# Kernel tuning notes

Hardware: AMD Instinct MI355X
Metric: run time of the kernel (lower is better)

Reference implementation:

```python
import jax, jax.numpy as jnp
import numpy as np

B, N = 2, 6
C_IN, C_OUT, D = 256, 80, 16
HF, WF = 32, 88
H_IN, W_IN = 256, 704
BEV_H, BEV_W = 128, 128
X_MIN, Y_MIN, Z_MIN, X_MAX, Y_MAX, Z_MAX = -51.2, -51.2, -5.0, 51.2, 51.2, 3.0
D_MIN, D_MAX = 0.0, 45.0
DX = (X_MAX - X_MIN) / BEV_W
DY = (Y_MAX - Y_MIN) / BEV_H


def _make_cameras():
    # Plausible surround-view rig: P = K [R|t], last row [0,0,0,1]
    K = np.array([[600., 0., W_IN / 2.], [0., 600., H_IN / 2.], [0., 0., 1.]])
    P = np.array([[0., -1., 0.], [0., 0., -1.], [1., 0., 0.]])  # lidar axes -> cam axes
    l2i = np.zeros((B, N, 4, 4), np.float32)
    for b in range(B):
        for n in range(N):
            th = 2 * np.pi * n / N + 0.05 * b
            Rz = np.array([[np.cos(-th), -np.sin(-th), 0.],
                           [np.sin(-th), np.cos(-th), 0.],
                           [0., 0., 1.]])
            Rc = P @ Rz
            c = np.array([1.5 * np.cos(th), 1.5 * np.sin(th), 1.6])  # camera center in lidar frame
            t = -Rc @ c
            M = np.eye(4)
            M[:3, :3] = K @ Rc
            M[:3, 3] = K @ t
            l2i[b, n] = M
    return jnp.asarray(l2i, dtype=jnp.float32)


def _make_aug():
    A = np.tile(np.eye(4, dtype=np.float32), (B, N, 1, 1))
    A[..., 0, 0] = 0.95
    A[..., 1, 1] = 0.95
    A[..., 0, 3] = 4.0
    A[..., 1, 3] = 2.0
    return jnp.asarray(A)


def setup_inputs() -> dict:
    key = jax.random.key(0)
    k = jax.random.split(key, 4)
    x = jax.random.normal(k[0], (B, N, C_IN, HF, WF), jnp.float32)
    w_dep = jax.random.normal(k[1], (D + C_OUT, C_IN), jnp.float32) * (1.0 / np.sqrt(C_IN))
    b_dep = jnp.zeros((D + C_OUT,), jnp.float32)
    w_ref = jax.random.normal(k[2], (C_OUT, C_OUT, 3, 3), jnp.float32) * (1.0 / np.sqrt(9.0 * C_OUT))
    b_ref = jnp.zeros((C_OUT,), jnp.float32)
    return {"x": x, "lidar2img": _make_cameras(), "img_aug": _make_aug(),
            "w_dep": w_dep, "b_dep": b_dep, "w_ref": w_ref, "b_ref": b_ref}


def _forward(x, lidar2img, img_aug, w_dep, b_dep, w_ref, b_ref):
    BN = B * N
    HW = HF * WF
    xf = x.reshape(BN, C_IN, HF, WF)
    # depthnet head: 1x1 conv -> D depth logits + C_OUT context channels
    y = jnp.einsum('oc,bchw->bohw', w_dep, xf) + b_dep[None, :, None, None]
    depth = jax.nn.softmax(y[:, :D], axis=1).reshape(BN, D, HW)   # (BN,D,HW)
    ctx = y[:, D:].reshape(BN, C_OUT, HW)                          # (BN,C,HW)

    # pixel-center grid in network-input image coords (as _make_pixel_grid)
    us = (jnp.arange(WF, dtype=jnp.float32) + 0.5) * (W_IN / WF)
    vs = (jnp.arange(HF, dtype=jnp.float32) + 0.5) * (H_IN / HF)
    vv, uu = jnp.meshgrid(vs, us, indexing='ij')
    uv1 = jnp.stack([uu, vv, jnp.ones_like(uu)], -1).reshape(HW, 3)

    # undo image augmentation: uv_raw = post_rot^-1 (uv1 - post_tran)
    aug = img_aug.reshape(BN, 4, 4)
    inv_rot = jnp.linalg.inv(aug[:, :3, :3])
    uv_raw = jnp.einsum('bij,bpj->bpi', inv_rot, uv1[None] - aug[:, None, :3, 3])  # (BN,HW,3)

    # unproject: X_lidar = lidar2img^-1 @ [u*d, v*d, d, 1]  (== R^-1(K^-1 d uv - t))
    inv_l2i = jnp.linalg.inv(lidar2img.reshape(BN, 4, 4))
    dvals = D_MIN + (jnp.arange(D, dtype=jnp.float32) + 0.5) * ((D_MAX - D_MIN) / D)
    pts_h = uv_raw[:, None, :, :] * dvals[None, :, None, None]                     # (BN,D,HW,3)
    pts = jnp.einsum('bij,bdpj->bdpi', inv_l2i[:, :3, :3], pts_h) + inv_l2i[:, None, None, :3, 3]

    ix = jnp.floor((pts[..., 0] - X_MIN) / DX).astype(jnp.int32)
    iy = jnp.floor((pts[..., 1] - Y_MIN) / DY).astype(jnp.int32)
    valid = (ix >= 0) & (ix < BEV_W) & (iy >= 0) & (iy < BEV_H) & \
            (pts[..., 2] >= Z_MIN) & (pts[..., 2] < Z_MAX)                          # (BN,D,HW)

    bidx = (jnp.arange(BN, dtype=jnp.int32) // N)[:, None, None]
    NUM = B * BEV_H * BEV_W
    flat = bidx * (BEV_H * BEV_W) + iy * BEV_W + ix
    flat = jnp.where(valid, flat, NUM).reshape(-1)  # invalid -> dump bucket

    # lift: per-point feature = depth_prob * context  -> splat (scatter-add) into BEV
    feat = depth[:, :, :, None] * jnp.swapaxes(ctx, 1, 2)[:, None, :, :]            # (BN,D,HW,C)
    acc = jax.ops.segment_sum(feat.reshape(-1, C_OUT), flat, num_segments=NUM + 1)[:NUM]
    cnt = jax.ops.segment_sum(jnp.ones_like(flat, dtype=jnp.float32), flat, num_segments=NUM + 1)[:NUM]
    acc = acc / jnp.maximum(cnt, 1.0)[:, None]  # normalize=True: average over points per cell

    bev = acc.reshape(B, BEV_H, BEV_W, C_OUT).transpose(0, 3, 1, 2)                 # (B,C,H,W)
    out = jax.lax.conv_general_dilated(bev, w_ref, (1, 1), 'SAME',
                                       dimension_numbers=('NCHW', 'OIHW', 'NCHW'))
    return out + b_ref[None, :, None, None]


def reference(x, lidar2img, img_aug, w_dep, b_dep, w_ref, b_ref):
    return _forward(x, lidar2img, img_aug, w_dep, b_dep, w_ref, b_ref)
```

## Files before the change

### kernel.cpp

```cpp
#include <hip/hip_runtime.h>
#include <math.h>

namespace {
constexpr int B_   = 2;
constexpr int NCAM = 6;
constexpr int BN   = 12;
constexpr int CIN  = 256;
constexpr int COUT = 80;
constexpr int DBIN = 16;
constexpr int NOUT = 96;
constexpr int HF = 32, WF = 88;
constexpr int HW = HF * WF;
constexpr int BEVH = 128, BEVW = 128;
constexpr int NUMC = B_ * BEVH * BEVW;
constexpr int NPTS = BN * DBIN * HW;

constexpr size_t MATS_OFF   = 0;
constexpr size_t WHI_OFF    = 2048;
constexpr size_t WLO_OFF    = WHI_OFF + 49152;
constexpr size_t YT_OFF     = 102400;
constexpr size_t CELL_OFF   = YT_OFF + 12976128;
constexpr size_t COUNTS_OFF = CELL_OFF + 2162688;
constexpr size_t STARTS_OFF = COUNTS_OFF + 131072;
constexpr size_t CURS_OFF   = STARTS_OFF + 131584;
constexpr size_t PLIST_OFF  = CURS_OFF + 131072;
constexpr size_t PCELL_OFF  = PLIST_OFF + 2162688;
constexpr size_t BEVHWC_OFF = PCELL_OFF + 2162688;
constexpr size_t WRH_OFF    = BEVHWC_OFF + 10485760;
constexpr size_t WRL_OFF    = WRH_OFF + 138240;
}

using bf16x8 = __attribute__((ext_vector_type(8))) short;
using f32x4  = __attribute__((ext_vector_type(4))) float;

__device__ inline unsigned short bf16rne(float f) {
    unsigned u = __float_as_uint(f);
    unsigned r = (u + 0x7FFFu + ((u >> 16) & 1u)) >> 16;
    return (unsigned short)r;
}

template<int NM>
__device__ void inv_lu_f32(float* A, float* Y) {
    int piv[NM];
    for (int j = 0; j < NM; j++) {
        int p = j; float mx = fabsf(A[j*NM+j]);
        for (int i = j+1; i < NM; i++) { float v = fabsf(A[i*NM+j]); if (v > mx) { mx = v; p = i; } }
        piv[j] = p;
        if (p != j) for (int k = 0; k < NM; k++) { float t = A[j*NM+k]; A[j*NM+k] = A[p*NM+k]; A[p*NM+k] = t; }
        float r = __fdiv_rn(1.0f, A[j*NM+j]);
        for (int i = j+1; i < NM; i++) A[i*NM+j] = __fmul_rn(A[i*NM+j], r);
        for (int i = j+1; i < NM; i++) {
            float lij = A[i*NM+j];
            for (int k = j+1; k < NM; k++)
                A[i*NM+k] = __fsub_rn(A[i*NM+k], __fmul_rn(lij, A[j*NM+k]));
        }
    }
    for (int c = 0; c < NM; c++) {
        float x[NM];
        for (int i = 0; i < NM; i++) x[i] = 0.f;
        x[c] = 1.f;
        for (int j = 0; j < NM; j++) { int p = piv[j]; if (p != j) { float t = x[j]; x[j] = x[p]; x[p] = t; } }
        for (int k = 0; k < NM; k++) {
            float xk = x[k];
            for (int i = k+1; i < NM; i++) x[i] = __fsub_rn(x[i], __fmul_rn(xk, A[i*NM+k]));
        }
        for (int k = NM-1; k >= 0; k--) {
            float xk = __fdiv_rn(x[k], A[k*NM+k]);
            x[k] = xk;
            for (int i = 0; i < k; i++) x[i] = __fsub_rn(x[i], __fmul_rn(xk, A[i*NM+k]));
        }
        for (int i = 0; i < NM; i++) Y[i*NM+c] = x[i];
    }
}

__global__ void lss_prep_kernel(const float* __restrict__ l2i,
                                const float* __restrict__ aug,
                                float* __restrict__ mats) {
    int n = threadIdx.x;
    if (n >= BN) return;
    float A[16], IA[16];
    for (int i = 0; i < 16; i++) A[i] = l2i[n*16 + i];
    inv_lu_f32<4>(A, IA);
    float R[9], IR[9];
    for (int i = 0; i < 3; i++)
        for (int j = 0; j < 3; j++) R[i*3+j] = aug[n*16 + i*4 + j];
    inv_lu_f32<3>(R, IR);
    float* o = mats + n*24;
    for (int i = 0; i < 9; i++) o[i] = IR[i];
    o[9]  = aug[n*16 + 3];
    o[10] = aug[n*16 + 7];
    o[11] = aug[n*16 + 11];
    for (int i = 0; i < 3; i++)
        for (int j = 0; j < 3; j++) o[12 + i*3 + j] = IA[i*4 + j];
    o[21] = IA[3]; o[22] = IA[7]; o[23] = IA[11];
}

__global__ void lss_wt_kernel(const float* __restrict__ w_dep,
                              unsigned short* __restrict__ wHi,
                              unsigned short* __restrict__ wLo) {
    int idx = blockIdx.x * 256 + threadIdx.x;
    float f = w_dep[idx];
    unsigned short h = bf16rne(f);
    float hf = __uint_as_float((unsigned)h << 16);
    wHi[idx] = h;
    wLo[idx] = bf16rne(f - hf);
}

__global__ void lss_wref_kernel(const float* __restrict__ w_ref,
                                unsigned short* __restrict__ wrh,
                                unsigned short* __restrict__ wrl) {
    int idx = blockIdx.x * 256 + threadIdx.x;
    int o  = idx / 864;
    int k  = idx - o * 864;
    int s  = k / 96;
    int ci = k - s * 96;
    float f = (ci < COUT) ? w_ref[(size_t)(o * COUT + ci) * 9 + s] : 0.f;
    unsigned short h = bf16rne(f);
    float hf = __uint_as_float((unsigned)h << 16);
    wrh[idx] = h;
    wrl[idx] = bf16rne(f - hf);
}

__global__ void lss_geom_kernel(const float* __restrict__ mats,
                                int* __restrict__ cellid,
                                int* __restrict__ counts) {
    int gp = blockIdx.x * 256 + threadIdx.x;
    int lane = threadIdx.x & 63;
    int bn = gp / HW, p = gp % HW;
    const float* m = mats + bn * 24;
    int ph = p / WF, pw = p % WF;
    float u = ((float)pw + 0.5f) * 8.0f;
    float v = ((float)ph + 0.5f) * 8.0f;
    float q0 = __fsub_rn(u, m[9]);
    float q1 = __fsub_rn(v, m[10]);
    float q2 = __fsub_rn(1.0f, m[11]);
    float r0 = __fadd_rn(__fadd_rn(__fmul_rn(m[0], q0), __fmul_rn(m[1], q1)), __fmul_rn(m[2], q2));
    float r1 = __fadd_rn(__fadd_rn(__fmul_rn(m[3], q0), __fmul_rn(m[4], q1)), __fmul_rn(m[5], q2));
    float r2 = __fadd_rn(__fadd_rn(__fmul_rn(m[6], q0), __fmul_rn(m[7], q1)), __fmul_rn(m[8], q2));
    int b = bn / NCAM;
    for (int d = 0; d < DBIN; d++) {
        float dv = __fmul_rn((float)d + 0.5f, 2.8125f);
        float p0 = __fmul_rn(r0, dv);
        float p1 = __fmul_rn(r1, dv);
        float p2 = __fmul_rn(r2, dv);
        float px = __fadd_rn(__fadd_rn(__fadd_rn(__fmul_rn(m[12], p0), __fmul_rn(m[13], p1)), __fmul_rn(m[14], p2)), m[21]);
        float py = __fadd_rn(__fadd_rn(__fadd_rn(__fmul_rn(m[15], p0), __fmul_rn(m[16], p1)), __fmul_rn(m[17], p2)), m[22]);
        float pz = __fadd_rn(__fadd_rn(__fadd_rn(__fmul_rn(m[18], p0), __fmul_rn(m[19], p1)), __fmul_rn(m[20], p2)), m[23]);
        float fx = floorf(__fdiv_rn(__fsub_rn(px, -51.2f), 0.8f));
        float fy = floorf(__fdiv_rn(__fsub_rn(py, -51.2f), 0.8f));
        int cell = -1;
        if (fx >= 0.0f && fx < 128.0f && fy >= 0.0f && fy < 128.0f && pz >= -5.0f && pz < 3.0f)
            cell = b * (BEVH * BEVW) + (int)fy * BEVW + (int)fx;
        cellid[(bn * DBIN + d) * HW + p] = cell;
        int cprev = __shfl_up(cell, 1);
        bool leader = (lane == 0) || (cell != cprev);
        unsigned long long L = __ballot(leader);
        unsigned long long above = (lane == 63) ? 0ull : (L >> (lane + 1));
        int runlen = above ? __ffsll(above) : (64 - lane);
        if (leader && cell >= 0) atomicAdd(&counts[cell], runlen);
    }
}

__global__ void lss_scan_kernel(const int* __restrict__ counts,
                                int* __restrict__ starts,
                                int* __restrict__ cursors) {
    __shared__ int sums[1024];
    int tid = threadIdx.x;
    int base = tid * 32;
    int local[32];
    int s = 0;
    #pragma unroll
    for (int i = 0; i < 32; i++) { local[i] = s; s += counts[base + i]; }
    sums[tid] = s;
    __syncthreads();
    for (int off = 1; off < 1024; off <<= 1) {
        int v = 0;
        if (tid >= off) v = sums[tid - off];
        __syncthreads();
        if (tid >= off) sums[tid] += v;
        __syncthreads();
    }
    int offset = (tid > 0) ? sums[tid - 1] : 0;
    #pragma unroll
    for (int i = 0; i < 32; i++) {
        int st = offset + local[i];
        starts[base + i]  = st;
        cursors[base + i] = st;
    }
    if (tid == 1023) starts[NUMC] = sums[1023];
}

__global__ void lss_fill_kernel(const int* __restrict__ cellid,
                                int* __restrict__ cursors,
                                int* __restrict__ plist,
                                int* __restrict__ pcell) {
    int i = blockIdx.x * 256 + threadIdx.x;
    int lane = threadIdx.x & 63;
    int c = cellid[i];
    int bn  = i / (DBIN * HW);
    int rem = i % (DBIN * HW);
    int d   = rem / HW;
    int p   = rem % HW;
    int pf  = ((bn * HW + p) << 4) | d;
    int cprev = __shfl_up(c, 1);
    bool leader = (lane == 0) || (c != cprev);
    unsigned long long L = __ballot(leader);
    unsigned long long above = (lane == 63) ? 0ull : (L >> (lane + 1));
    int runlen = above ? __ffsll(above) : (64 - lane);
    unsigned long long below = L & (~0ull >> (63 - lane));
    int lead = 63 - __clzll(below);
    int rank = lane - lead;
    int bse = 0;
    if (leader && c >= 0) bse = atomicAdd(&cursors[c], runlen);
    bse = __shfl(bse, lead);
    if (c >= 0) {
        plist[bse + rank] = pf;
        pcell[bse + rank] = c;
    }
}

__global__ __launch_bounds__(256) void lss_gemm_kernel(const float* __restrict__ x,
                                                       const unsigned short* __restrict__ wHi,
                                                       const unsigned short* __restrict__ wLo,
                                                       const float* __restrict__ b_dep,
                                                       float* __restrict__ yT) {
    __shared__ unsigned short xs[2][64][72];
    __shared__ unsigned short wsb[2][96][72];

    int tid  = threadIdx.x;
    int tl   = tid & 63;
    int tc   = tid >> 6;
    int pxg0 = blockIdx.x * 64;
    int bn   = pxg0 / HW;
    const float* xcol = x + (size_t)bn * CIN * HW + (pxg0 % HW) + tl;

    f32x4 acc[6];
    #pragma unroll
    for (int t = 0; t < 6; t++) acc[t] = (f32x4){0.f, 0.f, 0.f, 0.f};

    int lane = tid & 63;
    int wv   = tc;
    int n16  = lane & 15;
    int q    = lane >> 4;

    for (int k0 = 0; k0 < CIN; k0 += 64) {
        if (k0) __syncthreads();
        #pragma unroll 4
        for (int i = 0; i < 16; i++) {
            int kk = 4 * i + tc;
            float v = xcol[(size_t)(k0 + kk) * HW];
            unsigned short h = bf16rne(v);
            float hf = __uint_as_float((unsigned)h << 16);
            xs[0][tl][kk] = h;
            xs[1][tl][kk] = bf16rne(v - hf);
        }
        #pragma unroll
        for (int i = 0; i < 12; i++) {
            int idx = tid + i * 256;
            int plane = idx / 1536;
            int rem   = idx - plane * 1536;
            int o     = rem >> 4;
            int j     = rem & 15;
            const unsigned short* src = (plane ? wLo : wHi) + o * 256 + k0 + 4 * j;
            *(uint2*)&wsb[plane][o][4 * j] = *(const uint2*)src;
        }
        __syncthreads();
        #pragma unroll
        for (int ks = 0; ks < 64; ks += 32) {
            bf16x8 ah = *(const bf16x8*)&xs[0][16 * wv + n16][q * 8 + ks];
            bf16x8 al = *(const bf16x8*)&xs[1][16 * wv + n16][q * 8 + ks];
            #pragma unroll
            for (int t = 0; t < 6; t++) {
                bf16x8 bh = *(const bf16x8*)&wsb[0][16 * t + n16][q * 8 + ks];
                bf16x8 bl = *(const bf16x8*)&wsb[1][16 * t + n16][q * 8 + ks];
                acc[t] = __builtin_amdgcn_mfma_f32_16x16x32_bf16(ah, bh, acc[t], 0, 0, 0);
                acc[t] = __builtin_amdgcn_mfma_f32_16x16x32_bf16(ah, bl, acc[t], 0, 0, 0);
                acc[t] = __builtin_amdgcn_mfma_f32_16x16x32_bf16(al, bh, acc[t], 0, 0, 0);
            }
        }
    }

    float bias[6];
    #pragma unroll
    for (int t = 0; t < 6; t++) bias[t] = b_dep[16 * t + n16];
    #pragma unroll
    for (int r = 0; r < 4; r++) {
        int pxg = pxg0 + 16 * wv + 4 * q + r;
        float* yp = yT + (size_t)pxg * NOUT;
        float v0 = acc[0][r] + bias[0];
        float mx = v0;
        #pragma unroll
        for (int m = 1; m < 16; m <<= 1) mx = fmaxf(mx, __shfl_xor(mx, m));
        float e = expf(v0 - mx);
        float s = e;
        #pragma unroll
        for (int m = 1; m < 16; m <<= 1) s += __shfl_xor(s, m);
        yp[n16] = e / s;
        #pragma unroll
        for (int t = 1; t < 6; t++) yp[16 * t + n16] = acc[t][r] + bias[t];
    }
}

__global__ __launch_bounds__(256) void lss_gather_kernel(const float* __restrict__ yT,
                                                         const int* __restrict__ plist,
                                                         const int* __restrict__ pcell,
                                                         const int* __restrict__ nvptr,
                                                         float* __restrict__ bevHWC) {
    int wv   = threadIdx.x >> 6;
    int lane = threadIdx.x & 63;
    int pos0 = (blockIdx.x * 4 + wv) * 64;
    int nv = *nvptr;
    if (pos0 >= nv) return;
    int n = min(64, nv - pos0);
    int gp = pos0 + lane;
    int myp = (gp < nv) ? plist[gp] : 0;
    int myc = (gp < nv) ? pcell[gp] : -1;
    int l16 = lane & 15;

    float a0 = 0.f, a1 = 0.f;
    int cur = __shfl(myc, 0);
    int j = 0;
    for (; j + 4 <= n; j += 4) {
        int   pf[4], cc[4];
        float av[4], bv[4], dv[4];
        #pragma unroll
        for (int u = 0; u < 4; u++) {
            pf[u] = __shfl(myp, j + u);
            cc[u] = __shfl(myc, j + u);
        }
        #pragma unroll
        for (int u = 0; u < 4; u++) {
            const float* rp = yT + (size_t)(pf[u] >> 4) * NOUT;
            av[u] = rp[16 + lane];
            bv[u] = rp[80 + l16];
            dv[u] = rp[pf[u] & 15];
        }
        #pragma unroll
        for (int u = 0; u < 4; u++) {
            if (cc[u] != cur) {
                atomicAdd(&bevHWC[(size_t)cur * COUT + lane], a0);
                if (lane < 16) atomicAdd(&bevHWC[(size_t)cur * COUT + 64 + lane], a1);
                a0 = a1 = 0.f;
                cur = cc[u];
            }
            a0 = fmaf(dv[u], av[u], a0);
            a1 = fmaf(dv[u], bv[u], a1);
        }
    }
    for (; j < n; j++) {
        int pf = __shfl(myp, j);
        int c  = __shfl(myc, j);
        const float* rp = yT + (size_t)(pf >> 4) * NOUT;
        float aval = rp[16 + lane];
        float bval = rp[80 + l16];
        float dep  = rp[pf & 15];
        if (c != cur) {
            atomicAdd(&bevHWC[(size_t)cur * COUT + lane], a0);
            if (lane < 16) atomicAdd(&bevHWC[(size_t)cur * COUT + 64 + lane], a1);
            a0 = a1 = 0.f;
            cur = c;
        }
        a0 = fmaf(dep, aval, a0);
        a1 = fmaf(dep, bval, a1);
    }
    atomicAdd(&bevHWC[(size_t)cur * COUT + lane], a0);
    if (lane < 16) atomicAdd(&bevHWC[(size_t)cur * COUT + 64 + lane], a1);
}

__global__ __launch_bounds__(256) void lss_tr_kernel(const float* __restrict__ bevHWC,
                                                     const int* __restrict__ counts,
                                                     float* __restrict__ bevCHW) {
    __shared__ float t[COUT][65];
    __shared__ float ic[64];
    int tid = threadIdx.x;
    int cellbase = blockIdx.x * 64;
    if (tid < 64) {
        int cnt = counts[cellbase + tid];
        ic[tid] = 1.f / fmaxf((float)cnt, 1.f);
    }
    const float* src = bevHWC + (size_t)cellbase * COUT;
    #pragma unroll
    for (int k = 0; k < 20; k++) {
        int idx = tid + k * 256;
        int yx = idx / COUT, ch = idx % COUT;
        t[ch][yx] = src[idx];
    }
    __syncthreads();
    int b  = cellbase >> 14;
    int yx0 = cellbase & 16383;
    #pragma unroll
    for (int k = 0; k < 20; k++) {
        int idx = tid + k * 256;
        int ch = idx / 64, yxl = idx % 64;
        bevCHW[((size_t)(b * COUT + ch)) * (BEVH * BEVW) + yx0 + yxl] = t[ch][yxl] * ic[yxl];
    }
}

__global__ __launch_bounds__(256) void lss_conv_kernel(const float* __restrict__ bev,
                                                       const unsigned short* __restrict__ wrh,
                                                       const unsigned short* __restrict__ wrl,
                                                       const float* __restrict__ bias,
                                                       float* __restrict__ out) {
    __shared__ unsigned short inT[2][10][10][104];
    int tid = threadIdx.x;
    int blk = blockIdx.x;
    int b   = blk >> 8;
    int y0  = ((blk >> 4) & 15) * 8;
    int x0  = (blk & 15) * 8;
    int lane = tid & 63, w = tid >> 6;
    int q = lane >> 4, n16 = lane & 15;
    int ow = w >> 1;
    int pj = (w & 1) * 2;
    int pr = n16 >> 3, pc = n16 & 7;
    int NO = ow ? 2 : 3;
    int obase = ow * 48;
    int kq = 8 * q;
    int rowb0 = 2 * pj + pr;

    int woff[3];
    #pragma unroll
    for (int i = 0; i < 3; i++) woff[i] = (obase + 16 * i + n16) * 864 + kq;

    f32x4 acc[3][2];
    #pragma unroll
    for (int i = 0; i < 3; i++)
        #pragma unroll
        for (int j = 0; j < 2; j++) acc[i][j] = (f32x4){0.f, 0.f, 0.f, 0.f};

    const float* pb = bev + (size_t)b * COUT * (BEVH * BEVW);

    for (int cc = 0; cc < 3; cc++) {
        int ci0 = cc * 32;
        if (cc) __syncthreads();
        #pragma unroll
        for (int t = 0; t < 13; t++) {
            int idx = tid + t * 256;
            if (idx < 3200) {
                int ci  = idx / 100;
                int rem = idx - ci * 100;
                int r   = rem / 10;
                int c   = rem - r * 10;
                int gy = y0 + r - 1, gx = x0 + c - 1;
                int gci = ci0 + ci;
                float v = 0.f;
                if (gy >= 0 && gy < BEVH && gx >= 0 && gx < BEVW && gci < COUT)
                    v = pb[((size_t)gci * BEVH + gy) * BEVW + gx];
                unsigned short h = bf16rne(v);
                float hf = __uint_as_float((unsigned)h << 16);
                inT[0][r][c][ci] = h;
                inT[1][r][c][ci] = bf16rne(v - hf);
            }
        }
        __syncthreads();
        #pragma unroll
        for (int s = 0; s < 9; s++) {
            int dy = s / 3, dx = s - dy * 3;
            int kb = s * 96 + ci0;
            bf16x8 bh[2], bl[2];
            #pragma unroll
            for (int j = 0; j < 2; j++) {
                int rr = rowb0 + 2 * j + dy;
                int ccol = pc + dx;
                bh[j] = *(const bf16x8*)&inT[0][rr][ccol][kq];
                bl[j] = *(const bf16x8*)&inT[1][rr][ccol][kq];
            }
            #pragma unroll
            for (int i = 0; i < 3; i++) {
                if (i < NO) {
                    bf16x8 ah = *(const bf16x8*)&wrh[woff[i] + kb];
                    bf16x8 al = *(const bf16x8*)&wrl[woff[i] + kb];
                    #pragma unroll
                    for (int j = 0; j < 2; j++) {
                        acc[i][j] = __builtin_amdgcn_mfma_f32_16x16x32_bf16(ah, bh[j], acc[i][j], 0, 0, 0);
                        acc[i][j] = __builtin_amdgcn_mfma_f32_16x16x32_bf16(ah, bl[j], acc[i][j], 0, 0, 0);
                        acc[i][j] = __builtin_amdgcn_mfma_f32_16x16x32_bf16(al, bh[j], acc[i][j], 0, 0, 0);
                    }
                }
            }
        }
    }
    #pragma unroll
    for (int i = 0; i < 3; i++) {
        if (i < NO) {
            #pragma unroll
            for (int j = 0; j < 2; j++) {
                int gy = y0 + 2 * (pj + j) + pr;
                int gx = x0 + pc;
                #pragma unroll
                for (int r = 0; r < 4; r++) {
                    int o = obase + 16 * i + 4 * q + r;
                    out[((size_t)(b * COUT + o) * BEVH + gy) * BEVW + gx] = acc[i][j][r] + bias[o];
                }
            }
        }
    }
}

extern "C" void kernel_launch(void* const* d_in, const int* in_sizes, int n_in,
                              void* d_out, int out_size, void* d_ws, size_t ws_size,
                              hipStream_t stream) {
    (void)in_sizes; (void)n_in; (void)out_size; (void)ws_size;
    const float* x     = (const float*)d_in[0];
    const float* l2i   = (const float*)d_in[1];
    const float* aug   = (const float*)d_in[2];
    const float* w_dep = (const float*)d_in[3];
    const float* b_dep = (const float*)d_in[4];
    const float* w_ref = (const float*)d_in[5];
    const float* b_ref = (const float*)d_in[6];
    float* out = (float*)d_out;

    char* ws = (char*)d_ws;
    float* mats    = (float*)(ws + MATS_OFF);
    unsigned short* wHi = (unsigned short*)(ws + WHI_OFF);
    unsigned short* wLo = (unsigned short*)(ws + WLO_OFF);
    unsigned short* wrh = (unsigned short*)(ws + WRH_OFF);
    unsigned short* wrl = (unsigned short*)(ws + WRL_OFF);
    float* yT      = (float*)(ws + YT_OFF);
    float* bevCHW  = (float*)(ws + YT_OFF);
    int*   cellid  = (int*)(ws + CELL_OFF);
    int*   counts  = (int*)(ws + COUNTS_OFF);
    int*   starts  = (int*)(ws + STARTS_OFF);
    int*   cursors = (int*)(ws + CURS_OFF);
    int*   plist   = (int*)(ws + PLIST_OFF);
    int*   pcell   = (int*)(ws + PCELL_OFF);
    float* bevHWC  = (float*)(ws + BEVHWC_OFF);

    hipMemsetAsync(counts, 0, NUMC * sizeof(int), stream);
    hipMemsetAsync(bevHWC, 0, (size_t)NUMC * COUT * sizeof(float), stream);
    lss_prep_kernel<<<1, 64, 0, stream>>>(l2i, aug, mats);
    lss_wt_kernel<<<96, 256, 0, stream>>>(w_dep, wHi, wLo);
    lss_wref_kernel<<<270, 256, 0, stream>>>(w_ref, wrh, wrl);
    lss_geom_kernel<<<BN * HW / 256, 256, 0, stream>>>(mats, cellid, counts);
    lss_scan_kernel<<<1, 1024, 0, stream>>>(counts, starts, cursors);
    lss_fill_kernel<<<NPTS / 256, 256, 0, stream>>>(cellid, cursors, plist, pcell);
    lss_gemm_kernel<<<528, 256, 0, stream>>>(x, wHi, wLo, b_dep, yT);
    lss_gather_kernel<<<NPTS / 256, 256, 0, stream>>>(yT, plist, pcell, starts + NUMC, bevHWC);
    lss_tr_kernel<<<NUMC / 64, 256, 0, stream>>>(bevHWC, counts, bevCHW);
    lss_conv_kernel<<<512, 256, 0, stream>>>(bevCHW, wrh, wrl, b_ref, out);
}
```

Measured before the change: 233.9 us.

## Pre-split BEV into padded bf16 hi/lo HWC layout and read conv inputs from global

The transpose kernel now normalizes each cell, splits it into bf16 hi/lo halves, and writes a zero-padded 130x130 HWC layout with channels padded to 96. A memset clears the padding. The conv kernel drops its shared-memory staging, per-chunk conversion and barriers, and loads MFMA B operands directly from global/L2 in that layout. This removes the repeated halo conversion and the syncthreads in the conv. In exchange it adds an extra memset and uncoalesced-ish global vector loads that rely on caching, since neighbouring taps are reread.

Result: slower. 243.0 us (+3.9%).

```diff
diff --git a/kernel.cpp b/kernel.cpp
--- a/kernel.cpp
+++ b/kernel.cpp
@@ -14,6 +14,8 @@
 constexpr int BEVH = 128, BEVW = 128;
 constexpr int NUMC = B_ * BEVH * BEVW;
 constexpr int NPTS = BN * DBIN * HW;
+constexpr int PADG = 130;
+constexpr int PCELLS = PADG * PADG;
 
 constexpr size_t MATS_OFF   = 0;
 constexpr size_t WHI_OFF    = 2048;
@@ -28,6 +30,7 @@
 constexpr size_t BEVHWC_OFF = PCELL_OFF + 2162688;
 constexpr size_t WRH_OFF    = BEVHWC_OFF + 10485760;
 constexpr size_t WRL_OFF    = WRH_OFF + 138240;
+constexpr size_t BHWC16_BYTES = (size_t)B_ * 2 * PCELLS * 96 * 2;
 }
 
 using bf16x8 = __attribute__((ext_vector_type(8))) short;
@@ -369,8 +372,7 @@
 
 __global__ __launch_bounds__(256) void lss_tr_kernel(const float* __restrict__ bevHWC,
                                                      const int* __restrict__ counts,
-                                                     float* __restrict__ bevCHW) {
-    __shared__ float t[COUT][65];
+                                                     unsigned short* __restrict__ bhwc) {
     __shared__ float ic[64];
     int tid = threadIdx.x;
     int cellbase = blockIdx.x * 64;
@@ -378,30 +380,30 @@
         int cnt = counts[cellbase + tid];
         ic[tid] = 1.f / fmaxf((float)cnt, 1.f);
     }
-    const float* src = bevHWC + (size_t)cellbase * COUT;
-    #pragma unroll
-    for (int k = 0; k < 20; k++) {
-        int idx = tid + k * 256;
-        int yx = idx / COUT, ch = idx % COUT;
-        t[ch][yx] = src[idx];
-    }
     __syncthreads();
     int b  = cellbase >> 14;
-    int yx0 = cellbase & 16383;
-    #pragma unroll
-    for (int k = 0; k < 20; k++) {
+    int yx = cellbase & 16383;
+    int y = yx >> 7, x0 = yx & 127;
+    size_t padbase = (size_t)(b * 2) * PCELLS + (size_t)(y + 1) * PADG + (x0 + 1);
+    const float* src = bevHWC + (size_t)cellbase * COUT;
+    #pragma unroll
+    for (int k = 0; k < 24; k++) {
         int idx = tid + k * 256;
-        int ch = idx / 64, yxl = idx % 64;
-        bevCHW[((size_t)(b * COUT + ch)) * (BEVH * BEVW) + yx0 + yxl] = t[ch][yxl] * ic[yxl];
-    }
-}
-
-__global__ __launch_bounds__(256) void lss_conv_kernel(const float* __restrict__ bev,
+        int cl = idx / 96, ci = idx - cl * 96;
+        float v = (ci < COUT) ? src[cl * COUT + ci] * ic[cl] : 0.f;
+        unsigned short h = bf16rne(v);
+        float hf = __uint_as_float((unsigned)h << 16);
+        size_t o = (padbase + cl) * 96 + ci;
+        bhwc[o] = h;
+        bhwc[o + (size_t)PCELLS * 96] = bf16rne(v - hf);
+    }
+}
+
+__global__ __launch_bounds__(256) void lss_conv_kernel(const unsigned short* __restrict__ bhwc,
                                                        const unsigned short* __restrict__ wrh,
                                                        const unsigned short* __restrict__ wrl,
                                                        const float* __restrict__ bias,
                                                        float* __restrict__ out) {
-    __shared__ unsigned short inT[2][10][10][104];
     int tid = threadIdx.x;
     int blk = blockIdx.x;
     int b   = blk >> 8;
@@ -415,54 +417,36 @@
     int NO = ow ? 2 : 3;
     int obase = ow * 48;
     int kq = 8 * q;
-    int rowb0 = 2 * pj + pr;
 
     int woff[3];
     #pragma unroll
     for (int i = 0; i < 3; i++) woff[i] = (obase + 16 * i + n16) * 864 + kq;
 
+    const unsigned short* ph = bhwc + (size_t)(b * 2) * PCELLS * 96;
+    const unsigned short* pl = ph + (size_t)PCELLS * 96;
+    size_t rbase[2];
+    #pragma unroll
+    for (int j = 0; j < 2; j++)
+        rbase[j] = (size_t)(y0 + 2 * (pj + j) + pr) * PADG + (x0 + pc);
+
     f32x4 acc[3][2];
     #pragma unroll
     for (int i = 0; i < 3; i++)
         #pragma unroll
         for (int j = 0; j < 2; j++) acc[i][j] = (f32x4){0.f, 0.f, 0.f, 0.f};
 
-    const float* pb = bev + (size_t)b * COUT * (BEVH * BEVW);
-
-    for (int cc = 0; cc < 3; cc++) {
-        int ci0 = cc * 32;
-        if (cc) __syncthreads();
-        #pragma unroll
-        for (int t = 0; t < 13; t++) {
-            int idx = tid + t * 256;
-            if (idx < 3200) {
-                int ci  = idx / 100;
-                int rem = idx - ci * 100;
-                int r   = rem / 10;
-                int c   = rem - r * 10;
-                int gy = y0 + r - 1, gx = x0 + c - 1;
-                int gci = ci0 + ci;
-                float v = 0.f;
-                if (gy >= 0 && gy < BEVH && gx >= 0 && gx < BEVW && gci < COUT)
-                    v = pb[((size_t)gci * BEVH + gy) * BEVW + gx];
-                unsigned short h = bf16rne(v);
-                float hf = __uint_as_float((unsigned)h << 16);
-                inT[0][r][c][ci] = h;
-                inT[1][r][c][ci] = bf16rne(v - hf);
-            }
-        }
-        __syncthreads();
-        #pragma unroll
-        for (int s = 0; s < 9; s++) {
-            int dy = s / 3, dx = s - dy * 3;
-            int kb = s * 96 + ci0;
+    #pragma unroll
+    for (int s = 0; s < 9; s++) {
+        int dy = s / 3, dx = s - dy * 3;
+        #pragma unroll
+        for (int ks = 0; ks < 3; ks++) {
+            int kb = s * 96 + ks * 32;
             bf16x8 bh[2], bl[2];
             #pragma unroll
             for (int j = 0; j < 2; j++) {
-                int rr = rowb0 + 2 * j + dy;
-                int ccol = pc + dx;
-                bh[j] = *(const bf16x8*)&inT[0][rr][ccol][kq];
-                bl[j] = *(const bf16x8*)&inT[1][rr][ccol][kq];
+                size_t off = (rbase[j] + dy * PADG + dx) * 96 + ks * 32 + kq;
+                bh[j] = *(const bf16x8*)&ph[off];
+                bl[j] = *(const bf16x8*)&pl[off];
             }
             #pragma unroll
             for (int i = 0; i < 3; i++) {
@@ -516,7 +500,7 @@
     unsigned short* wrh = (unsigned short*)(ws + WRH_OFF);
     unsigned short* wrl = (unsigned short*)(ws + WRL_OFF);
     float* yT      = (float*)(ws + YT_OFF);
-    float* bevCHW  = (float*)(ws + YT_OFF);
+    unsigned short* bhwc16 = (unsigned short*)(ws + YT_OFF);
     int*   cellid  = (int*)(ws + CELL_OFF);
     int*   counts  = (int*)(ws + COUNTS_OFF);
     int*   starts  = (int*)(ws + STARTS_OFF);
@@ -535,6 +519,7 @@
     lss_fill_kernel<<<NPTS / 256, 256, 0, stream>>>(cellid, cursors, plist, pcell);
     lss_gemm_kernel<<<528, 256, 0, stream>>>(x, wHi, wLo, b_dep, yT);
     lss_gather_kernel<<<NPTS / 256, 256, 0, stream>>>(yT, plist, pcell, starts + NUMC, bevHWC);
-    lss_tr_kernel<<<NUMC / 64, 256, 0, stream>>>(bevHWC, counts, bevCHW);
-    lss_conv_kernel<<<512, 256, 0, stream>>>(bevCHW, wrh, wrl, b_ref, out);
-}
+    hipMemsetAsync(bhwc16, 0, BHWC16_BYTES, stream);
+    lss_tr_kernel<<<NUMC / 64, 256, 0, stream>>>(bevHWC, counts, bhwc16);
+    lss_conv_kernel<<<512, 256, 0, stream>>>(bhwc16, wrh, wrl, b_ref, out);
+}
```
